# Kernel tuning notes

Hardware: AMD Instinct MI355X
Metric: run time of the kernel (lower is better)

The kernel has to match this reference:

```python
import jax, jax.numpy as jnp
import numpy as np

NCLASS = 1000
H = 1.0
MIN_EPS = 1e-10
IGNORE_INDEX = -100


def setup_inputs() -> dict:
    key = jax.random.key(0)
    k1, k2, k3, k4 = jax.random.split(key, 4)
    N, M, D = 16384, 4096, 256
    return {
        "supp_embed": jax.random.normal(k1, (N, D), dtype=jnp.float32),
        "pred_embed": jax.random.normal(k2, (M, D), dtype=jnp.float32),
        "supp_target": jax.random.randint(k3, (N,), 0, NCLASS, dtype=jnp.int64)
        if jax.config.jax_enable_x64 else jax.random.randint(k3, (N,), 0, NCLASS, dtype=jnp.int32),
        "target": jax.random.randint(k4, (M,), 0, NCLASS, dtype=jnp.int32),
    }


def _kde_ce(supp_embed, pred_embed, supp_target, target):
    d = supp_embed.shape[1]
    sq = (jnp.sum(pred_embed * pred_embed, axis=1, keepdims=True)
          + jnp.sum(supp_embed * supp_embed, axis=1)[None, :]
          - 2.0 * pred_embed @ supp_embed.T)
    sq = jnp.maximum(sq, 0.0)
    K = jnp.exp(sq / (-d * H))                      # RBF kernel, (M, N)
    # drop_max is False here (X_pred provided, not LOO); weights = 1.0
    K = K / jnp.clip(jnp.sum(K, axis=1, keepdims=True), MIN_EPS)
    Y = jax.nn.one_hot(supp_target, NCLASS, dtype=K.dtype)  # (N, K)
    pred = K @ Y                                    # class probabilities (M, K)
    # LogLoss: NLL on probabilities with ignore_index + mean reduction
    valid = target != IGNORE_INDEX
    safe_t = jnp.where(valid, target, 0)
    p = jnp.take_along_axis(pred, safe_t[:, None], axis=1)[:, 0]
    nll = -jnp.log(jnp.clip(p, MIN_EPS))
    loss = jnp.sum(nll * valid) / jnp.maximum(jnp.sum(valid), 1)
    return loss, pred


def reference(supp_embed, pred_embed, supp_target, target):
    loss, pred = _kde_ce(supp_embed, pred_embed, supp_target, target)
    return loss
```

## Files before the change

kernel.cpp:

```cpp
#include <hip/hip_runtime.h>
#include <hip/hip_bf16.h>

typedef __bf16 bf16x8 __attribute__((ext_vector_type(8)));
typedef float  f32x4  __attribute__((ext_vector_type(4)));
typedef short  short8 __attribute__((ext_vector_type(8)));

#define KDE_IGNORE (-100)
#define GS   8
#define GBM  64
#define GBN  64
#define GD   256

__device__ __forceinline__ f32x4 mfma16x16(bf16x8 a, bf16x8 b, f32x4 c) {
  return __builtin_amdgcn_mfma_f32_16x16x32_bf16(a, b, c, 0, 0, 0);
}

template<bool CONV>
__global__ void supp_prep_kernel(const float* __restrict__ supp, float* __restrict__ sn,
                                 short* __restrict__ suppB, int N) {
  int row = blockIdx.x * 8 + ((threadIdx.x >> 6) << 1) + ((threadIdx.x & 63) >> 5);
  int c = threadIdx.x & 31;
  const float* src = supp + (size_t)row * GD + c * 8;
  float4 a = *reinterpret_cast<const float4*>(src);
  float4 b = *reinterpret_cast<const float4*>(src + 4);
  if (CONV) {
    union { short8 v; __bf16 h[8]; } u;
    u.h[0] = (__bf16)a.x; u.h[1] = (__bf16)a.y; u.h[2] = (__bf16)a.z; u.h[3] = (__bf16)a.w;
    u.h[4] = (__bf16)b.x; u.h[5] = (__bf16)b.y; u.h[6] = (__bf16)b.z; u.h[7] = (__bf16)b.w;
    *reinterpret_cast<short8*>(suppB + (size_t)row * GD + c * 8) = u.v;
  }
  float s = a.x*a.x + a.y*a.y + a.z*a.z + a.w*a.w
          + b.x*b.x + b.y*b.y + b.z*b.z + b.w*b.w;
#pragma unroll
  for (int off = 16; off >= 1; off >>= 1) s += __shfl_xor(s, off, 32);
  if (c == 0) sn[row] = s;
}

template<bool PRE>
__device__ __forceinline__ short8 load_chunk(const float* suppF, const short* suppB,
                                             int row, int j) {
  if (PRE) {
    return *reinterpret_cast<const short8*>(suppB + (size_t)row * GD + j * 8);
  } else {
    const float* p = suppF + (size_t)row * GD + j * 8;
    float4 a = *reinterpret_cast<const float4*>(p);
    float4 b = *reinterpret_cast<const float4*>(p + 4);
    union { short8 v; __bf16 h[8]; } u;
    u.h[0] = (__bf16)a.x; u.h[1] = (__bf16)a.y; u.h[2] = (__bf16)a.z; u.h[3] = (__bf16)a.w;
    u.h[4] = (__bf16)b.x; u.h[5] = (__bf16)b.y; u.h[6] = (__bf16)b.z; u.h[7] = (__bf16)b.w;
    return u.v;
  }
}

template<bool PRE>
__global__ __launch_bounds__(256, 2)
void kde_gemm_kernel(const float* __restrict__ pred, const float* __restrict__ suppF,
                     const short* __restrict__ suppB,
                     const int* __restrict__ tgt, const int* __restrict__ suppT,
                     const float* __restrict__ sn,
                     float* __restrict__ denomP, float* __restrict__ numerP,
                     int M, int N) {
  __shared__ __align__(16) short Bs[2][GBN * GD];

  const int bid = blockIdx.x;
  const int mb  = bid >> 3;
  const int s   = bid & 7;
  const int m0  = mb * GBM;
  const int nslice = N >> 3;
  const int nbase  = s * nslice;
  const int niter  = nslice / GBN;
  const int t    = threadIdx.x;
  const int lane = t & 63;
  const int wid  = t >> 6;
  const int wm   = (wid >> 1) * 32;
  const int wnl  = (wid & 1) * 32;
  const int lr = lane >> 4, lc = lane & 15;

  bf16x8 af[2][8];
#pragma unroll
  for (int mt = 0; mt < 2; ++mt) {
    const float* base = pred + (size_t)(m0 + wm + mt * 16 + lc) * GD + lr * 8;
#pragma unroll
    for (int kk = 0; kk < 8; ++kk) {
      float4 a = *reinterpret_cast<const float4*>(base + kk * 32);
      float4 b = *reinterpret_cast<const float4*>(base + kk * 32 + 4);
      union { bf16x8 v; __bf16 h[8]; } u;
      u.h[0] = (__bf16)a.x; u.h[1] = (__bf16)a.y; u.h[2] = (__bf16)a.z; u.h[3] = (__bf16)a.w;
      u.h[4] = (__bf16)b.x; u.h[5] = (__bf16)b.y; u.h[6] = (__bf16)b.z; u.h[7] = (__bf16)b.w;
      af[mt][kk] = u.v;
    }
  }
  int tmv[2][4];
#pragma unroll
  for (int mt = 0; mt < 2; ++mt)
#pragma unroll
    for (int rg = 0; rg < 4; ++rg)
      tmv[mt][rg] = tgt[m0 + wm + mt * 16 + lr * 4 + rg];

  float dac[2][4] = {}, nac[2][4] = {};

#pragma unroll
  for (int i = 0; i < 8; ++i) {
    int C = i * 256 + t; int row = C >> 5; int j = C & 31;
    short8 v = load_chunk<PRE>(suppF, suppB, nbase + row, j);
    *reinterpret_cast<short8*>(&Bs[0][row * GD + ((j ^ (row & 31)) << 3)]) = v;
  }
  __syncthreads();

  const float SC  = 1.4426950408889634f / 128.0f;
  const float SCH = 1.4426950408889634f / 256.0f;

  for (int it = 0; it < niter; ++it) {
    const int cur = it & 1;
    const int n0 = nbase + it * GBN;
    const bool more = (it + 1 < niter);

    short8 sreg[8];
    if (more) {
      const int n1 = n0 + GBN;
#pragma unroll
      for (int i = 0; i < 8; ++i) {
        int C = i * 256 + t; int row = C >> 5; int j = C & 31;
        sreg[i] = load_chunk<PRE>(suppF, suppB, n1 + row, j);
      }
    }
    float snv[2]; int stv[2];
#pragma unroll
    for (int nt = 0; nt < 2; ++nt) {
      int j = n0 + wnl + nt * 16 + lc;
      snv[nt] = sn[j]; stv[nt] = suppT[j];
    }

    f32x4 acc[2][2] = {};
    __builtin_amdgcn_s_setprio(1);
#pragma unroll
    for (int ks = 0; ks < 8; ++ks) {
      bf16x8 bf[2];
#pragma unroll
      for (int nt = 0; nt < 2; ++nt) {
        int r = wnl + nt * 16 + lc;
        int cs = (ks * 4 + lr) ^ (r & 31);
        bf[nt] = *reinterpret_cast<const bf16x8*>(&Bs[cur][r * GD + (cs << 3)]);
      }
#pragma unroll
      for (int mt = 0; mt < 2; ++mt)
#pragma unroll
        for (int nt = 0; nt < 2; ++nt)
          acc[mt][nt] = mfma16x16(af[mt][ks], bf[nt], acc[mt][nt]);
    }
    __builtin_amdgcn_s_setprio(0);

    if (more) {
#pragma unroll
      for (int i = 0; i < 8; ++i) {
        int C = i * 256 + t; int row = C >> 5; int j = C & 31;
        *reinterpret_cast<short8*>(&Bs[cur ^ 1][row * GD + ((j ^ (row & 31)) << 3)]) = sreg[i];
      }
    }

#pragma unroll
    for (int nt = 0; nt < 2; ++nt) {
      float sh = -snv[nt] * SCH;
#pragma unroll
      for (int mt = 0; mt < 2; ++mt)
#pragma unroll
        for (int rg = 0; rg < 4; ++rg) {
          float e = exp2f(fmaf(acc[mt][nt][rg], SC, sh));
          dac[mt][rg] += e;
          nac[mt][rg] += (stv[nt] == tmv[mt][rg]) ? e : 0.0f;
        }
    }
    __syncthreads();
  }

#pragma unroll
  for (int off = 1; off < 16; off <<= 1) {
#pragma unroll
    for (int mt = 0; mt < 2; ++mt)
#pragma unroll
      for (int rg = 0; rg < 4; ++rg) {
        dac[mt][rg] += __shfl_xor(dac[mt][rg], off);
        nac[mt][rg] += __shfl_xor(nac[mt][rg], off);
      }
  }
  if (lc == 0) {
    const int slot = s * 2 + (wid & 1);
#pragma unroll
    for (int mt = 0; mt < 2; ++mt)
#pragma unroll
      for (int rg = 0; rg < 4; ++rg) {
        int m = m0 + wm + mt * 16 + lr * 4 + rg;
        denomP[(size_t)slot * M + m] = dac[mt][rg];
        numerP[(size_t)slot * M + m] = nac[mt][rg];
      }
  }
}

__global__ void kde_reduce_kernel(const float* __restrict__ denomP, const float* __restrict__ numerP,
                                  const int* __restrict__ tgt,
                                  float* __restrict__ bsum, float* __restrict__ bcnt, int M) {
  __shared__ float sS[4], sC[4];
  int m = blockIdx.x * 256 + threadIdx.x;
  float den = 0.0f, num = 0.0f;
#pragma unroll
  for (int sl = 0; sl < 16; ++sl) {
    den += denomP[(size_t)sl * M + m];
    num += numerP[(size_t)sl * M + m];
  }
  int tg = tgt[m];
  bool valid = (tg != KDE_IGNORE);
  float p = fmaxf(num / fmaxf(den, 1e-10f), 1e-10f);
  float nll = valid ? -logf(p) : 0.0f;
  float cnt = valid ? 1.0f : 0.0f;
#pragma unroll
  for (int off = 32; off >= 1; off >>= 1) {
    nll += __shfl_xor(nll, off);
    cnt += __shfl_xor(cnt, off);
  }
  int wid = threadIdx.x >> 6, lane = threadIdx.x & 63;
  if (lane == 0) { sS[wid] = nll; sC[wid] = cnt; }
  __syncthreads();
  if (threadIdx.x == 0) {
    bsum[blockIdx.x] = sS[0] + sS[1] + sS[2] + sS[3];
    bcnt[blockIdx.x] = sC[0] + sC[1] + sC[2] + sC[3];
  }
}

__global__ void kde_final_kernel(const float* __restrict__ bsum, const float* __restrict__ bcnt,
                                 float* __restrict__ out, int nb) {
  int tid = threadIdx.x;
  float s = (tid < nb) ? bsum[tid] : 0.0f;
  float c = (tid < nb) ? bcnt[tid] : 0.0f;
#pragma unroll
  for (int off = 32; off >= 1; off >>= 1) {
    s += __shfl_xor(s, off);
    c += __shfl_xor(c, off);
  }
  if (tid == 0) out[0] = s / fmaxf(c, 1.0f);
}

extern "C" void kernel_launch(void* const* d_in, const int* in_sizes, int n_in,
                              void* d_out, int out_size, void* d_ws, size_t ws_size,
                              hipStream_t stream) {
  const float* supp  = (const float*)d_in[0];
  const float* pred  = (const float*)d_in[1];
  const int*   suppT = (const int*)d_in[2];
  const int*   tgt   = (const int*)d_in[3];
  const int N = in_sizes[2];
  const int M = in_sizes[3];

  float* sn     = (float*)d_ws;
  float* denomP = sn + N;
  float* numerP = denomP + 16 * (size_t)M;
  float* bsum   = numerP + 16 * (size_t)M;
  float* bcnt   = bsum + 16;
  short* suppB  = (short*)(bcnt + 16);

  size_t small = sizeof(float) * ((size_t)N + 32 * (size_t)M + 32);
  bool pre = ws_size >= small + sizeof(short) * (size_t)N * GD;

  if (pre) supp_prep_kernel<true ><<<dim3(N / 8), dim3(256), 0, stream>>>(supp, sn, suppB, N);
  else     supp_prep_kernel<false><<<dim3(N / 8), dim3(256), 0, stream>>>(supp, sn, nullptr, N);

  dim3 grid((M / GBM) * GS);
  if (pre) kde_gemm_kernel<true ><<<grid, dim3(256), 0, stream>>>(
      pred, supp, suppB, tgt, suppT, sn, denomP, numerP, M, N);
  else     kde_gemm_kernel<false><<<grid, dim3(256), 0, stream>>>(
      pred, supp, suppB, tgt, suppT, sn, denomP, numerP, M, N);

  kde_reduce_kernel<<<dim3(M / 256), dim3(256), 0, stream>>>(denomP, numerP, tgt, bsum, bcnt, M);
  kde_final_kernel<<<dim3(1), dim3(64), 0, stream>>>(bsum, bcnt, (float*)d_out, M / 256);
}
```

Before: 76.40 us.

## Use 512-thread blocks with 128-row M tiles and 16 N slices

The GEMM kernel now uses 8 waves per block covering 128 query rows, so each staged support tile in shared memory feeds twice as many rows. The N dimension is split into 16 slices instead of 8, which keeps the grid at 512 blocks and doubles the partial-result slots the reduce kernel must sum. Launch bounds move to (512,4), which limits registers per thread for the preloaded A fragments and may cause spills. The chunk-loading helper is inlined and the cur buffer index is toggled explicitly.

```diff
diff --git a/kernel.cpp b/kernel.cpp
--- a/kernel.cpp
+++ b/kernel.cpp
@@ -6,10 +6,11 @@
 typedef short  short8 __attribute__((ext_vector_type(8)));
 
 #define KDE_IGNORE (-100)
-#define GS   8
-#define GBM  64
+#define NSL  16
+#define GBM  128
 #define GBN  64
 #define GD   256
+#define NSLOT (NSL * 2)
 
 __device__ __forceinline__ f32x4 mfma16x16(bf16x8 a, bf16x8 b, f32x4 c) {
   return __builtin_amdgcn_mfma_f32_16x16x32_bf16(a, b, c, 0, 0, 0);
@@ -37,23 +38,7 @@
 }
 
 template<bool PRE>
-__device__ __forceinline__ short8 load_chunk(const float* suppF, const short* suppB,
-                                             int row, int j) {
-  if (PRE) {
-    return *reinterpret_cast<const short8*>(suppB + (size_t)row * GD + j * 8);
-  } else {
-    const float* p = suppF + (size_t)row * GD + j * 8;
-    float4 a = *reinterpret_cast<const float4*>(p);
-    float4 b = *reinterpret_cast<const float4*>(p + 4);
-    union { short8 v; __bf16 h[8]; } u;
-    u.h[0] = (__bf16)a.x; u.h[1] = (__bf16)a.y; u.h[2] = (__bf16)a.z; u.h[3] = (__bf16)a.w;
-    u.h[4] = (__bf16)b.x; u.h[5] = (__bf16)b.y; u.h[6] = (__bf16)b.z; u.h[7] = (__bf16)b.w;
-    return u.v;
-  }
-}
-
-template<bool PRE>
-__global__ __launch_bounds__(256, 2)
+__global__ __launch_bounds__(512, 4)
 void kde_gemm_kernel(const float* __restrict__ pred, const float* __restrict__ suppF,
                      const short* __restrict__ suppB,
                      const int* __restrict__ tgt, const int* __restrict__ suppT,
@@ -63,17 +48,18 @@
   __shared__ __align__(16) short Bs[2][GBN * GD];
 
   const int bid = blockIdx.x;
-  const int mb  = bid >> 3;
-  const int s   = bid & 7;
+  const int mb  = bid >> 4;
+  const int s   = bid & 15;
   const int m0  = mb * GBM;
-  const int nslice = N >> 3;
+  const int nslice = N >> 4;
   const int nbase  = s * nslice;
   const int niter  = nslice / GBN;
   const int t    = threadIdx.x;
   const int lane = t & 63;
   const int wid  = t >> 6;
   const int wm   = (wid >> 1) * 32;
-  const int wnl  = (wid & 1) * 32;
+  const int wng  = wid & 1;
+  const int wnl  = wng * 32;
   const int lr = lane >> 4, lc = lane & 15;
 
   bf16x8 af[2][8];
@@ -99,29 +85,49 @@
 
   float dac[2][4] = {}, nac[2][4] = {};
 
-#pragma unroll
-  for (int i = 0; i < 8; ++i) {
-    int C = i * 256 + t; int row = C >> 5; int j = C & 31;
-    short8 v = load_chunk<PRE>(suppF, suppB, nbase + row, j);
-    *reinterpret_cast<short8*>(&Bs[0][row * GD + ((j ^ (row & 31)) << 3)]) = v;
-  }
-  __syncthreads();
-
   const float SC  = 1.4426950408889634f / 128.0f;
   const float SCH = 1.4426950408889634f / 256.0f;
 
+#pragma unroll
+  for (int i = 0; i < 4; ++i) {
+    int C = i * 512 + t; int row = C >> 5; int j = C & 31;
+    short8 v;
+    if (PRE) {
+      v = *reinterpret_cast<const short8*>(suppB + (size_t)(nbase + row) * GD + j * 8);
+    } else {
+      const float* p = suppF + (size_t)(nbase + row) * GD + j * 8;
+      float4 a = *reinterpret_cast<const float4*>(p);
+      float4 b = *reinterpret_cast<const float4*>(p + 4);
+      union { short8 v8; __bf16 h[8]; } u;
+      u.h[0] = (__bf16)a.x; u.h[1] = (__bf16)a.y; u.h[2] = (__bf16)a.z; u.h[3] = (__bf16)a.w;
+      u.h[4] = (__bf16)b.x; u.h[5] = (__bf16)b.y; u.h[6] = (__bf16)b.z; u.h[7] = (__bf16)b.w;
+      v = u.v8;
+    }
+    *reinterpret_cast<short8*>(&Bs[0][row * GD + ((j ^ (row & 31)) << 3)]) = v;
+  }
+  __syncthreads();
+
+  int cur = 0;
   for (int it = 0; it < niter; ++it) {
-    const int cur = it & 1;
     const int n0 = nbase + it * GBN;
     const bool more = (it + 1 < niter);
 
-    short8 sreg[8];
+    short8 sreg[4];
     if (more) {
-      const int n1 = n0 + GBN;
-#pragma unroll
-      for (int i = 0; i < 8; ++i) {
-        int C = i * 256 + t; int row = C >> 5; int j = C & 31;
-        sreg[i] = load_chunk<PRE>(suppF, suppB, n1 + row, j);
+#pragma unroll
+      for (int i = 0; i < 4; ++i) {
+        int C = i * 512 + t; int row = C >> 5; int j = C & 31;
+        if (PRE) {
+          sreg[i] = *reinterpret_cast<const short8*>(suppB + (size_t)(n0 + GBN + row) * GD + j * 8);
+        } else {
+          const float* p = suppF + (size_t)(n0 + GBN + row) * GD + j * 8;
+          float4 a = *reinterpret_cast<const float4*>(p);
+          float4 b = *reinterpret_cast<const float4*>(p + 4);
+          union { short8 v8; __bf16 h[8]; } u;
+          u.h[0] = (__bf16)a.x; u.h[1] = (__bf16)a.y; u.h[2] = (__bf16)a.z; u.h[3] = (__bf16)a.w;
+          u.h[4] = (__bf16)b.x; u.h[5] = (__bf16)b.y; u.h[6] = (__bf16)b.z; u.h[7] = (__bf16)b.w;
+          sreg[i] = u.v8;
+        }
       }
     }
     float snv[2]; int stv[2];
@@ -135,25 +141,25 @@
     __builtin_amdgcn_s_setprio(1);
 #pragma unroll
     for (int ks = 0; ks < 8; ++ks) {
-      bf16x8 bf[2];
+      bf16x8 bfr[2];
 #pragma unroll
       for (int nt = 0; nt < 2; ++nt) {
         int r = wnl + nt * 16 + lc;
         int cs = (ks * 4 + lr) ^ (r & 31);
-        bf[nt] = *reinterpret_cast<const bf16x8*>(&Bs[cur][r * GD + (cs << 3)]);
+        bfr[nt] = *reinterpret_cast<const bf16x8*>(&Bs[cur][r * GD + (cs << 3)]);
       }
 #pragma unroll
       for (int mt = 0; mt < 2; ++mt)
 #pragma unroll
         for (int nt = 0; nt < 2; ++nt)
-          acc[mt][nt] = mfma16x16(af[mt][ks], bf[nt], acc[mt][nt]);
+          acc[mt][nt] = mfma16x16(af[mt][ks], bfr[nt], acc[mt][nt]);
     }
     __builtin_amdgcn_s_setprio(0);
 
     if (more) {
 #pragma unroll
-      for (int i = 0; i < 8; ++i) {
-        int C = i * 256 + t; int row = C >> 5; int j = C & 31;
+      for (int i = 0; i < 4; ++i) {
+        int C = i * 512 + t; int row = C >> 5; int j = C & 31;
         *reinterpret_cast<short8*>(&Bs[cur ^ 1][row * GD + ((j ^ (row & 31)) << 3)]) = sreg[i];
       }
     }
@@ -171,6 +177,7 @@
         }
     }
     __syncthreads();
+    cur ^= 1;
   }
 
 #pragma unroll
@@ -184,7 +191,7 @@
       }
   }
   if (lc == 0) {
-    const int slot = s * 2 + (wid & 1);
+    const int slot = s * 2 + wng;
 #pragma unroll
     for (int mt = 0; mt < 2; ++mt)
 #pragma unroll
@@ -203,7 +210,7 @@
   int m = blockIdx.x * 256 + threadIdx.x;
   float den = 0.0f, num = 0.0f;
 #pragma unroll
-  for (int sl = 0; sl < 16; ++sl) {
+  for (int sl = 0; sl < NSLOT; ++sl) {
     den += denomP[(size_t)sl * M + m];
     num += numerP[(size_t)sl * M + m];
   }
@@ -251,21 +258,21 @@
 
   float* sn     = (float*)d_ws;
   float* denomP = sn + N;
-  float* numerP = denomP + 16 * (size_t)M;
-  float* bsum   = numerP + 16 * (size_t)M;
+  float* numerP = denomP + (size_t)NSLOT * M;
+  float* bsum   = numerP + (size_t)NSLOT * M;
   float* bcnt   = bsum + 16;
   short* suppB  = (short*)(bcnt + 16);
 
-  size_t small = sizeof(float) * ((size_t)N + 32 * (size_t)M + 32);
+  size_t small = sizeof(float) * ((size_t)N + 2 * (size_t)NSLOT * M + 32);
   bool pre = ws_size >= small + sizeof(short) * (size_t)N * GD;
 
   if (pre) supp_prep_kernel<true ><<<dim3(N / 8), dim3(256), 0, stream>>>(supp, sn, suppB, N);
   else     supp_prep_kernel<false><<<dim3(N / 8), dim3(256), 0, stream>>>(supp, sn, nullptr, N);
 
-  dim3 grid((M / GBM) * GS);
-  if (pre) kde_gemm_kernel<true ><<<grid, dim3(256), 0, stream>>>(
+  dim3 grid((M / GBM) * NSL);
+  if (pre) kde_gemm_kernel<true ><<<grid, dim3(512), 0, stream>>>(
       pred, supp, suppB, tgt, suppT, sn, denomP, numerP, M, N);
-  else     kde_gemm_kernel<false><<<grid, dim3(256), 0, stream>>>(
+  else     kde_gemm_kernel<false><<<grid, dim3(512), 0, stream>>>(
       pred, supp, suppB, tgt, suppT, sn, denomP, numerP, M, N);
 
   kde_reduce_kernel<<<dim3(M / 256), dim3(256), 0, stream>>>(denomP, numerP, tgt, bsum, bcnt, M);
```

Result: slower. 155.6 us (+103.7%).
